# Kernel tuning notes

Measured on AMD Instinct MI355X. Metric: run time of the kernel, lower is better.

Reference implementation:

```python
import jax, jax.numpy as jnp
import numpy as np

N_HID, N_HEAD, N_K, N_V = 1024, 16, 64, 64
B, S = 2, 2048


def setup_inputs() -> dict:
    key = jax.random.key(0)
    ks = jax.random.split(key, 5)
    w_scale = 1.0 / np.sqrt(N_HID)  # keep pre-softmax logits in a sane range
    x = jax.random.normal(ks[0], (B, S, N_HID), dtype=jnp.float32)
    mask = jax.random.randint(ks[1], (B, S, N_HEAD, S), 0, 2) > 0  # [B, Sq, H, Sk] bool
    W_qkv = jax.random.normal(ks[2], (N_HID, N_HEAD * (2 * N_K + N_V)), dtype=jnp.float32) * w_scale
    b_qkv = jnp.zeros((N_HEAD * (2 * N_K + N_V),), dtype=jnp.float32)
    W_out = jax.random.normal(ks[3], (N_HEAD * N_V, N_HID), dtype=jnp.float32) * w_scale
    b_out = jnp.zeros((N_HID,), dtype=jnp.float32)
    return {"x": x, "mask": mask, "W_qkv": W_qkv, "b_qkv": b_qkv, "W_out": W_out, "b_out": b_out}


def reference(x, mask, W_qkv, b_qkv, W_out, b_out):
    nb, sl, nh = x.shape
    qkv = x @ W_qkv + b_qkv                                  # [B, S, H*(2k+v)]
    qkv = qkv.reshape(nb, sl, N_HEAD, 2 * N_K + N_V).transpose(0, 2, 1, 3)  # [B, H, S, 2k+v]
    q, k, v = qkv[..., :N_K], qkv[..., N_K:2 * N_K], qkv[..., 2 * N_K:]
    qk = jnp.einsum('bhqd,bhkd->bhqk', q, k) / np.sqrt(N_K)  # [B, H, Sq, Sk]
    # original masks on the [B, Sq, H, Sk] view; swap mask axes instead of qk
    mask_bhqk = jnp.swapaxes(mask, 1, 2)                     # [B, H, Sq, Sk]
    qk = jnp.where(mask_bhqk, qk, -jnp.inf)
    attn = jax.nn.softmax(qk, axis=-1)
    ctx = jnp.einsum('bhqk,bhkd->bhqd', attn, v)             # [B, H, S, n_v]
    ctx = ctx.transpose(0, 2, 1, 3).reshape(nb, sl, N_HEAD * N_V)
    out = ctx @ W_out + b_out
    return x + out
```

## Files before the change

kernel.cpp:

```cpp
#include <hip/hip_runtime.h>

#define SEQ 2048
#define NHEAD 16
#define NHID 1024

typedef __attribute__((ext_vector_type(8))) short bf16x8;
typedef __attribute__((ext_vector_type(4))) float f32x4;
typedef unsigned short u16;

__device__ inline u16 f2bf(float f) {
    union { float f; unsigned u; } v; v.f = f;
    unsigned r = v.u + 0x7FFFu + ((v.u >> 16) & 1u);
    return (u16)(r >> 16);
}

__global__ void cast_kernel(const float* __restrict__ in, u16* __restrict__ out, int n4) {
    int i = blockIdx.x * 256 + threadIdx.x;
    if (i < n4) {
        float4 v = ((const float4*)in)[i];
        ushort4 o;
        o.x = f2bf(v.x); o.y = f2bf(v.y); o.z = f2bf(v.z); o.w = f2bf(v.w);
        ((ushort4*)out)[i] = o;
    }
}

__global__ void transpose_cast(const float* __restrict__ in, u16* __restrict__ out, int R, int C) {
    __shared__ float tile[32][33];
    int bx = blockIdx.x * 32, by = blockIdx.y * 32;
    int tx = threadIdx.x & 31, ty = threadIdx.x >> 5;
#pragma unroll
    for (int i = ty; i < 32; i += 8) tile[i][tx] = in[(size_t)(by + i) * C + bx + tx];
    __syncthreads();
#pragma unroll
    for (int i = ty; i < 32; i += 8) out[(size_t)(bx + i) * R + by + tx] = f2bf(tile[tx][i]);
}

__launch_bounds__(256, 2)
__global__ void gemm_qkv(const u16* __restrict__ A, const u16* __restrict__ Bt,
                         const float* __restrict__ bias,
                         u16* __restrict__ qs, u16* __restrict__ ks, u16* __restrict__ vs) {
    __shared__ __align__(16) u16 Alds[128 * 72];
    __shared__ __align__(16) u16 Blds[128 * 72];
    const int tid = threadIdx.x;
    const int m0 = blockIdx.y * 128, n0 = blockIdx.x * 128;
    const int lane = tid & 63, wid = tid >> 6;
    const int wm = (wid & 1) * 64, wn = (wid >> 1) * 64;
    const int col = lane & 15, quad = lane >> 4;
    const int sr = tid >> 3, scg = (tid & 7) * 8;
    f32x4 acc[4][4] = {};
    for (int k0 = 0; k0 < 1024; k0 += 64) {
#pragma unroll
        for (int p = 0; p < 4; p++) {
            int r = sr + p * 32;
            *(bf16x8*)&Alds[r * 72 + scg] = *(const bf16x8*)&A[(size_t)(m0 + r) * 1024 + k0 + scg];
            *(bf16x8*)&Blds[r * 72 + scg] = *(const bf16x8*)&Bt[(size_t)(n0 + r) * 1024 + k0 + scg];
        }
        __syncthreads();
#pragma unroll
        for (int kc = 0; kc < 2; kc++) {
            bf16x8 af[4], bfr[4];
#pragma unroll
            for (int t = 0; t < 4; t++) {
                af[t]  = *(const bf16x8*)&Alds[(wm + t * 16 + col) * 72 + kc * 32 + quad * 8];
                bfr[t] = *(const bf16x8*)&Blds[(wn + t * 16 + col) * 72 + kc * 32 + quad * 8];
            }
#pragma unroll
            for (int mt = 0; mt < 4; mt++)
#pragma unroll
                for (int nt = 0; nt < 4; nt++)
                    acc[mt][nt] = __builtin_amdgcn_mfma_f32_16x16x32_bf16(af[mt], bfr[nt], acc[mt][nt], 0, 0, 0);
        }
        __syncthreads();
    }
#pragma unroll
    for (int mt = 0; mt < 4; mt++)
#pragma unroll
        for (int nt = 0; nt < 4; nt++)
#pragma unroll
            for (int r = 0; r < 4; r++) {
                int gm = m0 + wm + mt * 16 + quad * 4 + r;
                int gn = n0 + wn + nt * 16 + col;
                float val = acc[mt][nt][r] + bias[gn];
                int b = gm >> 11, s = gm & 2047;
                int h = gn / 192, rr = gn - h * 192;
                size_t base = ((size_t)(b * NHEAD + h) * SEQ + s) * 64;
                if (rr < 64)        qs[base + rr] = f2bf(val * 0.125f);
                else if (rr < 128)  ks[base + rr - 64] = f2bf(val);
                else                vs[base + rr - 128] = f2bf(val);
            }
}

__launch_bounds__(256, 2)
__global__ void attn_kernel(const u16* __restrict__ qs, const u16* __restrict__ ks,
                            const u16* __restrict__ vs, const int* __restrict__ mask,
                            u16* __restrict__ ctx) {
    __shared__ __align__(16) u16 Klds[64 * 72];
    __shared__ __align__(16) u16 Vt[64 * 72];
    __shared__ __align__(16) u16 Plds[4][16 * 72];
    const int tid = threadIdx.x;
    const int lane = tid & 63, wid = tid >> 6;
    const int col = lane & 15, quad = lane >> 4;
    const int bh = blockIdx.y;
    const int b = bh >> 4, h = bh & 15;
    const int q0 = blockIdx.x * 64;
    const size_t hbase = (size_t)bh * SEQ * 64;

    const u16* qp = qs + hbase + (size_t)(q0 + wid * 16 + col) * 64 + quad * 8;
    bf16x8 aq0 = *(const bf16x8*)qp;
    bf16x8 aq1 = *(const bf16x8*)(qp + 32);

    float m_i[4], l_i[4], alpha[4];
    f32x4 O[4] = {};
#pragma unroll
    for (int r = 0; r < 4; r++) { m_i[r] = -INFINITY; l_i[r] = 0.f; }

    const int sr = tid >> 3, scg = (tid & 7) * 8;
    for (int kb = 0; kb < SEQ; kb += 64) {
        __syncthreads();
#pragma unroll
        for (int p = 0; p < 2; p++) {
            int r = sr + p * 32;
            *(bf16x8*)&Klds[r * 72 + scg] = *(const bf16x8*)&ks[hbase + (size_t)(kb + r) * 64 + scg];
            bf16x8 vv = *(const bf16x8*)&vs[hbase + (size_t)(kb + r) * 64 + scg];
#pragma unroll
            for (int j = 0; j < 8; j++) Vt[(scg + j) * 72 + r] = (u16)vv[j];
        }
        __syncthreads();

        f32x4 sacc[4];
#pragma unroll
        for (int nt = 0; nt < 4; nt++) {
            bf16x8 b0 = *(const bf16x8*)&Klds[(nt * 16 + col) * 72 + quad * 8];
            bf16x8 b1 = *(const bf16x8*)&Klds[(nt * 16 + col) * 72 + 32 + quad * 8];
            f32x4 z = {};
            z = __builtin_amdgcn_mfma_f32_16x16x32_bf16(aq0, b0, z, 0, 0, 0);
            z = __builtin_amdgcn_mfma_f32_16x16x32_bf16(aq1, b1, z, 0, 0, 0);
            sacc[nt] = z;
        }
        float sv[4][4];
#pragma unroll
        for (int nt = 0; nt < 4; nt++)
#pragma unroll
            for (int r = 0; r < 4; r++) {
                int q = q0 + wid * 16 + quad * 4 + r;
                int key = kb + nt * 16 + col;
                int mv = mask[(((size_t)b * SEQ + q) * NHEAD + h) * SEQ + key];
                sv[nt][r] = mv ? sacc[nt][r] : -1e30f;
            }
#pragma unroll
        for (int r = 0; r < 4; r++) {
            float rm = fmaxf(fmaxf(sv[0][r], sv[1][r]), fmaxf(sv[2][r], sv[3][r]));
            rm = fmaxf(rm, __shfl_xor(rm, 1));
            rm = fmaxf(rm, __shfl_xor(rm, 2));
            rm = fmaxf(rm, __shfl_xor(rm, 4));
            rm = fmaxf(rm, __shfl_xor(rm, 8));
            float mnew = fmaxf(m_i[r], rm);
            alpha[r] = __expf(m_i[r] - mnew);
            m_i[r] = mnew;
        }
        float rsum[4] = {0.f, 0.f, 0.f, 0.f};
#pragma unroll
        for (int nt = 0; nt < 4; nt++)
#pragma unroll
            for (int r = 0; r < 4; r++) {
                float p = __expf(sv[nt][r] - m_i[r]);
                rsum[r] += p;
                Plds[wid][(quad * 4 + r) * 72 + nt * 16 + col] = f2bf(p);
            }
#pragma unroll
        for (int r = 0; r < 4; r++) {
            float rs = rsum[r];
            rs += __shfl_xor(rs, 1);
            rs += __shfl_xor(rs, 2);
            rs += __shfl_xor(rs, 4);
            rs += __shfl_xor(rs, 8);
            l_i[r] = l_i[r] * alpha[r] + rs;
        }
#pragma unroll
        for (int dt = 0; dt < 4; dt++)
#pragma unroll
            for (int r = 0; r < 4; r++) O[dt][r] *= alpha[r];
        __syncthreads();

        bf16x8 ap0 = *(const bf16x8*)&Plds[wid][col * 72 + quad * 8];
        bf16x8 ap1 = *(const bf16x8*)&Plds[wid][col * 72 + 32 + quad * 8];
#pragma unroll
        for (int dt = 0; dt < 4; dt++) {
            bf16x8 bv0 = *(const bf16x8*)&Vt[(dt * 16 + col) * 72 + quad * 8];
            bf16x8 bv1 = *(const bf16x8*)&Vt[(dt * 16 + col) * 72 + 32 + quad * 8];
            O[dt] = __builtin_amdgcn_mfma_f32_16x16x32_bf16(ap0, bv0, O[dt], 0, 0, 0);
            O[dt] = __builtin_amdgcn_mfma_f32_16x16x32_bf16(ap1, bv1, O[dt], 0, 0, 0);
        }
    }
#pragma unroll
    for (int dt = 0; dt < 4; dt++)
#pragma unroll
        for (int r = 0; r < 4; r++) {
            float val = O[dt][r] / l_i[r];
            int q = q0 + wid * 16 + quad * 4 + r;
            int c = h * 64 + dt * 16 + col;
            ctx[(size_t)(b * SEQ + q) * NHID + c] = f2bf(val);
        }
}

__launch_bounds__(256, 2)
__global__ void gemm_out(const u16* __restrict__ A, const u16* __restrict__ Bt,
                         const float* __restrict__ bias, const float* __restrict__ xres,
                         float* __restrict__ out) {
    __shared__ __align__(16) u16 Alds[128 * 72];
    __shared__ __align__(16) u16 Blds[128 * 72];
    const int tid = threadIdx.x;
    const int m0 = blockIdx.y * 128, n0 = blockIdx.x * 128;
    const int lane = tid & 63, wid = tid >> 6;
    const int wm = (wid & 1) * 64, wn = (wid >> 1) * 64;
    const int col = lane & 15, quad = lane >> 4;
    const int sr = tid >> 3, scg = (tid & 7) * 8;
    f32x4 acc[4][4] = {};
    for (int k0 = 0; k0 < 1024; k0 += 64) {
#pragma unroll
        for (int p = 0; p < 4; p++) {
            int r = sr + p * 32;
            *(bf16x8*)&Alds[r * 72 + scg] = *(const bf16x8*)&A[(size_t)(m0 + r) * 1024 + k0 + scg];
            *(bf16x8*)&Blds[r * 72 + scg] = *(const bf16x8*)&Bt[(size_t)(n0 + r) * 1024 + k0 + scg];
        }
        __syncthreads();
#pragma unroll
        for (int kc = 0; kc < 2; kc++) {
            bf16x8 af[4], bfr[4];
#pragma unroll
            for (int t = 0; t < 4; t++) {
                af[t]  = *(const bf16x8*)&Alds[(wm + t * 16 + col) * 72 + kc * 32 + quad * 8];
                bfr[t] = *(const bf16x8*)&Blds[(wn + t * 16 + col) * 72 + kc * 32 + quad * 8];
            }
#pragma unroll
            for (int mt = 0; mt < 4; mt++)
#pragma unroll
                for (int nt = 0; nt < 4; nt++)
                    acc[mt][nt] = __builtin_amdgcn_mfma_f32_16x16x32_bf16(af[mt], bfr[nt], acc[mt][nt], 0, 0, 0);
        }
        __syncthreads();
    }
#pragma unroll
    for (int mt = 0; mt < 4; mt++)
#pragma unroll
        for (int nt = 0; nt < 4; nt++)
#pragma unroll
            for (int r = 0; r < 4; r++) {
                int gm = m0 + wm + mt * 16 + quad * 4 + r;
                int gn = n0 + wn + nt * 16 + col;
                out[(size_t)gm * NHID + gn] = acc[mt][nt][r] + bias[gn] + xres[(size_t)gm * NHID + gn];
            }
}

extern "C" void kernel_launch(void* const* d_in, const int* in_sizes, int n_in,
                              void* d_out, int out_size, void* d_ws, size_t ws_size,
                              hipStream_t stream) {
    const float* x     = (const float*)d_in[0];
    const int*   mask  = (const int*)d_in[1];
    const float* W_qkv = (const float*)d_in[2];
    const float* b_qkv = (const float*)d_in[3];
    const float* W_out = (const float*)d_in[4];
    const float* b_out = (const float*)d_in[5];
    float* out = (float*)d_out;

    char* ws = (char*)d_ws;
    u16* x_bf   = (u16*)(ws);
    u16* wqkv_t = (u16*)(ws + (size_t)(8  << 20));
    u16* wout_t = (u16*)(ws + (size_t)(14 << 20));
    u16* qs     = (u16*)(ws + (size_t)(16 << 20));
    u16* ks     = (u16*)(ws + (size_t)(24 << 20));
    u16* vs     = (u16*)(ws + (size_t)(32 << 20));
    u16* ctx    = (u16*)(ws + (size_t)(40 << 20));

    cast_kernel<<<4096, 256, 0, stream>>>(x, x_bf, 4096 * 1024 / 4);
    transpose_cast<<<dim3(3072 / 32, 1024 / 32), 256, 0, stream>>>(W_qkv, wqkv_t, 1024, 3072);
    transpose_cast<<<dim3(1024 / 32, 1024 / 32), 256, 0, stream>>>(W_out, wout_t, 1024, 1024);
    gemm_qkv<<<dim3(24, 32), 256, 0, stream>>>(x_bf, wqkv_t, b_qkv, qs, ks, vs);
    attn_kernel<<<dim3(32, 32), 256, 0, stream>>>(qs, ks, vs, mask, ctx);
    gemm_out<<<dim3(8, 32), 256, 0, stream>>>(ctx, wout_t, b_out, x, out);
}
```

Measured before the change: 877.5 us.

## Store V transposed, read K/V directly from global in attention, use global_load_lds in GEMMs

The QKV GEMM now writes V in a transposed [bh, d, seq] layout, so the attention kernel no longer stages K and V through LDS with a scalar transpose. Instead each wave reads its MFMA operands straight from global memory (leaning on L2/L1), which removes two block-wide barriers per key tile. Mask pointers are precomputed per row. Both GEMMs switch to direct global-to-LDS loads with an unpadded 64-wide LDS row, which can bring back LDS bank conflicts on the fragment reads. The transposed V stores in the QKV epilogue are strided and may cost extra write bandwidth.

After: 940.8 us. 1.07x slower.

```diff
diff --git a/kernel.cpp b/kernel.cpp
--- a/kernel.cpp
+++ b/kernel.cpp
@@ -12,6 +12,14 @@
     union { float f; unsigned u; } v; v.f = f;
     unsigned r = v.u + 0x7FFFu + ((v.u >> 16) & 1u);
     return (u16)(r >> 16);
+}
+
+typedef __attribute__((address_space(3))) unsigned int  lds_uint;
+typedef const __attribute__((address_space(1))) unsigned int glob_uint;
+__device__ __forceinline__ void gl2lds16(const void* g, void* l) {
+    __builtin_amdgcn_global_load_lds((glob_uint*)(unsigned long long)g,
+                                     (lds_uint*)(unsigned int)(unsigned long long)l,
+                                     16, 0, 0);
 }
 
 __global__ void cast_kernel(const float* __restrict__ in, u16* __restrict__ out, int n4) {
@@ -38,9 +46,9 @@
 __launch_bounds__(256, 2)
 __global__ void gemm_qkv(const u16* __restrict__ A, const u16* __restrict__ Bt,
                          const float* __restrict__ bias,
-                         u16* __restrict__ qs, u16* __restrict__ ks, u16* __restrict__ vs) {
-    __shared__ __align__(16) u16 Alds[128 * 72];
-    __shared__ __align__(16) u16 Blds[128 * 72];
+                         u16* __restrict__ qs, u16* __restrict__ ks, u16* __restrict__ vt) {
+    __shared__ __align__(16) u16 Alds[128 * 64];
+    __shared__ __align__(16) u16 Blds[128 * 64];
     const int tid = threadIdx.x;
     const int m0 = blockIdx.y * 128, n0 = blockIdx.x * 128;
     const int lane = tid & 63, wid = tid >> 6;
@@ -52,8 +60,8 @@
 #pragma unroll
         for (int p = 0; p < 4; p++) {
             int r = sr + p * 32;
-            *(bf16x8*)&Alds[r * 72 + scg] = *(const bf16x8*)&A[(size_t)(m0 + r) * 1024 + k0 + scg];
-            *(bf16x8*)&Blds[r * 72 + scg] = *(const bf16x8*)&Bt[(size_t)(n0 + r) * 1024 + k0 + scg];
+            gl2lds16(&A[(size_t)(m0 + r) * 1024 + k0 + scg], &Alds[(p * 32 + wid * 8) * 64]);
+            gl2lds16(&Bt[(size_t)(n0 + r) * 1024 + k0 + scg], &Blds[(p * 32 + wid * 8) * 64]);
         }
         __syncthreads();
 #pragma unroll
@@ -61,8 +69,8 @@
             bf16x8 af[4], bfr[4];
 #pragma unroll
             for (int t = 0; t < 4; t++) {
-                af[t]  = *(const bf16x8*)&Alds[(wm + t * 16 + col) * 72 + kc * 32 + quad * 8];
-                bfr[t] = *(const bf16x8*)&Blds[(wn + t * 16 + col) * 72 + kc * 32 + quad * 8];
+                af[t]  = *(const bf16x8*)&Alds[(wm + t * 16 + col) * 64 + kc * 32 + quad * 8];
+                bfr[t] = *(const bf16x8*)&Blds[(wn + t * 16 + col) * 64 + kc * 32 + quad * 8];
             }
 #pragma unroll
             for (int mt = 0; mt < 4; mt++)
@@ -83,55 +91,48 @@
                 float val = acc[mt][nt][r] + bias[gn];
                 int b = gm >> 11, s = gm & 2047;
                 int h = gn / 192, rr = gn - h * 192;
-                size_t base = ((size_t)(b * NHEAD + h) * SEQ + s) * 64;
-                if (rr < 64)        qs[base + rr] = f2bf(val * 0.125f);
-                else if (rr < 128)  ks[base + rr - 64] = f2bf(val);
-                else                vs[base + rr - 128] = f2bf(val);
+                size_t bh = (size_t)(b * NHEAD + h);
+                if (rr < 64)       qs[(bh * SEQ + s) * 64 + rr] = f2bf(val * 0.125f);
+                else if (rr < 128) ks[(bh * SEQ + s) * 64 + rr - 64] = f2bf(val);
+                else               vt[(bh * 64 + rr - 128) * SEQ + s] = f2bf(val);
             }
 }
 
 __launch_bounds__(256, 2)
 __global__ void attn_kernel(const u16* __restrict__ qs, const u16* __restrict__ ks,
-                            const u16* __restrict__ vs, const int* __restrict__ mask,
+                            const u16* __restrict__ vt, const int* __restrict__ mask,
                             u16* __restrict__ ctx) {
-    __shared__ __align__(16) u16 Klds[64 * 72];
-    __shared__ __align__(16) u16 Vt[64 * 72];
     __shared__ __align__(16) u16 Plds[4][16 * 72];
     const int tid = threadIdx.x;
     const int lane = tid & 63, wid = tid >> 6;
     const int col = lane & 15, quad = lane >> 4;
-    const int bh = blockIdx.y;
-    const int b = bh >> 4, h = bh & 15;
-    const int q0 = blockIdx.x * 64;
+    const int bh = blockIdx.y, b = bh >> 4, h = bh & 15;
+    const int q0 = blockIdx.x * 64 + wid * 16;
     const size_t hbase = (size_t)bh * SEQ * 64;
 
-    const u16* qp = qs + hbase + (size_t)(q0 + wid * 16 + col) * 64 + quad * 8;
+    const u16* qp = qs + hbase + (size_t)(q0 + col) * 64 + quad * 8;
     bf16x8 aq0 = *(const bf16x8*)qp;
     bf16x8 aq1 = *(const bf16x8*)(qp + 32);
 
+    const int* mp[4];
+#pragma unroll
+    for (int r = 0; r < 4; r++)
+        mp[r] = mask + (((size_t)b * SEQ + (q0 + quad * 4 + r)) * NHEAD + h) * SEQ + col;
+
+    const u16* kbase = ks + hbase + (size_t)col * 64 + quad * 8;
+    const u16* vbase = vt + ((size_t)bh * 64 + col) * SEQ + quad * 8;
+
     float m_i[4], l_i[4], alpha[4];
     f32x4 O[4] = {};
 #pragma unroll
     for (int r = 0; r < 4; r++) { m_i[r] = -INFINITY; l_i[r] = 0.f; }
 
-    const int sr = tid >> 3, scg = (tid & 7) * 8;
     for (int kb = 0; kb < SEQ; kb += 64) {
-        __syncthreads();
-#pragma unroll
-        for (int p = 0; p < 2; p++) {
-            int r = sr + p * 32;
-            *(bf16x8*)&Klds[r * 72 + scg] = *(const bf16x8*)&ks[hbase + (size_t)(kb + r) * 64 + scg];
-            bf16x8 vv = *(const bf16x8*)&vs[hbase + (size_t)(kb + r) * 64 + scg];
-#pragma unroll
-            for (int j = 0; j < 8; j++) Vt[(scg + j) * 72 + r] = (u16)vv[j];
-        }
-        __syncthreads();
-
         f32x4 sacc[4];
 #pragma unroll
         for (int nt = 0; nt < 4; nt++) {
-            bf16x8 b0 = *(const bf16x8*)&Klds[(nt * 16 + col) * 72 + quad * 8];
-            bf16x8 b1 = *(const bf16x8*)&Klds[(nt * 16 + col) * 72 + 32 + quad * 8];
+            bf16x8 b0 = *(const bf16x8*)(kbase + (size_t)(kb + nt * 16) * 64);
+            bf16x8 b1 = *(const bf16x8*)(kbase + (size_t)(kb + nt * 16) * 64 + 32);
             f32x4 z = {};
             z = __builtin_amdgcn_mfma_f32_16x16x32_bf16(aq0, b0, z, 0, 0, 0);
             z = __builtin_amdgcn_mfma_f32_16x16x32_bf16(aq1, b1, z, 0, 0, 0);
@@ -141,12 +142,8 @@
 #pragma unroll
         for (int nt = 0; nt < 4; nt++)
 #pragma unroll
-            for (int r = 0; r < 4; r++) {
-                int q = q0 + wid * 16 + quad * 4 + r;
-                int key = kb + nt * 16 + col;
-                int mv = mask[(((size_t)b * SEQ + q) * NHEAD + h) * SEQ + key];
-                sv[nt][r] = mv ? sacc[nt][r] : -1e30f;
-            }
+            for (int r = 0; r < 4; r++)
+                sv[nt][r] = mp[r][kb + nt * 16] ? sacc[nt][r] : -1e30f;
 #pragma unroll
         for (int r = 0; r < 4; r++) {
             float rm = fmaxf(fmaxf(sv[0][r], sv[1][r]), fmaxf(sv[2][r], sv[3][r]));
@@ -180,14 +177,13 @@
         for (int dt = 0; dt < 4; dt++)
 #pragma unroll
             for (int r = 0; r < 4; r++) O[dt][r] *= alpha[r];
-        __syncthreads();
 
         bf16x8 ap0 = *(const bf16x8*)&Plds[wid][col * 72 + quad * 8];
         bf16x8 ap1 = *(const bf16x8*)&Plds[wid][col * 72 + 32 + quad * 8];
 #pragma unroll
         for (int dt = 0; dt < 4; dt++) {
-            bf16x8 bv0 = *(const bf16x8*)&Vt[(dt * 16 + col) * 72 + quad * 8];
-            bf16x8 bv1 = *(const bf16x8*)&Vt[(dt * 16 + col) * 72 + 32 + quad * 8];
+            bf16x8 bv0 = *(const bf16x8*)(vbase + (size_t)(dt * 16) * SEQ + kb);
+            bf16x8 bv1 = *(const bf16x8*)(vbase + (size_t)(dt * 16) * SEQ + kb + 32);
             O[dt] = __builtin_amdgcn_mfma_f32_16x16x32_bf16(ap0, bv0, O[dt], 0, 0, 0);
             O[dt] = __builtin_amdgcn_mfma_f32_16x16x32_bf16(ap1, bv1, O[dt], 0, 0, 0);
         }
@@ -197,9 +193,8 @@
 #pragma unroll
         for (int r = 0; r < 4; r++) {
             float val = O[dt][r] / l_i[r];
-            int q = q0 + wid * 16 + quad * 4 + r;
-            int c = h * 64 + dt * 16 + col;
-            ctx[(size_t)(b * SEQ + q) * NHID + c] = f2bf(val);
+            int q = q0 + quad * 4 + r;
+            ctx[(size_t)(b * SEQ + q) * NHID + h * 64 + dt * 16 + col] = f2bf(val);
         }
 }
 
@@ -207,8 +202,8 @@
 __global__ void gemm_out(const u16* __restrict__ A, const u16* __restrict__ Bt,
                          const float* __restrict__ bias, const float* __restrict__ xres,
                          float* __restrict__ out) {
-    __shared__ __align__(16) u16 Alds[128 * 72];
-    __shared__ __align__(16) u16 Blds[128 * 72];
+    __shared__ __align__(16) u16 Alds[128 * 64];
+    __shared__ __align__(16) u16 Blds[128 * 64];
     const int tid = threadIdx.x;
     const int m0 = blockIdx.y * 128, n0 = blockIdx.x * 128;
     const int lane = tid & 63, wid = tid >> 6;
@@ -220,8 +215,8 @@
 #pragma unroll
         for (int p = 0; p < 4; p++) {
             int r = sr + p * 32;
-            *(bf16x8*)&Alds[r * 72 + scg] = *(const bf16x8*)&A[(size_t)(m0 + r) * 1024 + k0 + scg];
-            *(bf16x8*)&Blds[r * 72 + scg] = *(const bf16x8*)&Bt[(size_t)(n0 + r) * 1024 + k0 + scg];
+            gl2lds16(&A[(size_t)(m0 + r) * 1024 + k0 + scg], &Alds[(p * 32 + wid * 8) * 64]);
+            gl2lds16(&Bt[(size_t)(n0 + r) * 1024 + k0 + scg], &Blds[(p * 32 + wid * 8) * 64]);
         }
         __syncthreads();
 #pragma unroll
@@ -229,8 +224,8 @@
             bf16x8 af[4], bfr[4];
 #pragma unroll
             for (int t = 0; t < 4; t++) {
-                af[t]  = *(const bf16x8*)&Alds[(wm + t * 16 + col) * 72 + kc * 32 + quad * 8];
-                bfr[t] = *(const bf16x8*)&Blds[(wn + t * 16 + col) * 72 + kc * 32 + quad * 8];
+                af[t]  = *(const bf16x8*)&Alds[(wm + t * 16 + col) * 64 + kc * 32 + quad * 8];
+                bfr[t] = *(const bf16x8*)&Blds[(wn + t * 16 + col) * 64 + kc * 32 + quad * 8];
             }
 #pragma unroll
             for (int mt = 0; mt < 4; mt++)
@@ -269,13 +264,13 @@
     u16* wout_t = (u16*)(ws + (size_t)(14 << 20));
     u16* qs     = (u16*)(ws + (size_t)(16 << 20));
     u16* ks     = (u16*)(ws + (size_t)(24 << 20));
-    u16* vs     = (u16*)(ws + (size_t)(32 << 20));
+    u16* vt     = (u16*)(ws + (size_t)(32 << 20));
     u16* ctx    = (u16*)(ws + (size_t)(40 << 20));
 
     cast_kernel<<<4096, 256, 0, stream>>>(x, x_bf, 4096 * 1024 / 4);
     transpose_cast<<<dim3(3072 / 32, 1024 / 32), 256, 0, stream>>>(W_qkv, wqkv_t, 1024, 3072);
     transpose_cast<<<dim3(1024 / 32, 1024 / 32), 256, 0, stream>>>(W_out, wout_t, 1024, 1024);
-    gemm_qkv<<<dim3(24, 32), 256, 0, stream>>>(x_bf, wqkv_t, b_qkv, qs, ks, vs);
-    attn_kernel<<<dim3(32, 32), 256, 0, stream>>>(qs, ks, vs, mask, ctx);
+    gemm_qkv<<<dim3(24, 32), 256, 0, stream>>>(x_bf, wqkv_t, b_qkv, qs, ks, vt);
+    attn_kernel<<<dim3(32, 32), 256, 0, stream>>>(qs, ks, vt, mask, ctx);
     gemm_out<<<dim3(8, 32), 256, 0, stream>>>(ctx, wout_t, b_out, x, out);
 }
```
